# Performance work log

Hardware: AMD Instinct MI355X
Metric: run time of the kernel (lower is better)

The kernel has to match this reference:

```python
import jax, jax.numpy as jnp
import numpy as np

IN_DIM = 512
E = 512            # embed_dim
DI = 1024          # d_inner = expand * embed_dim
S = 16             # d_state
DC = 4             # d_conv
DT_RANK = 32       # ceil(embed_dim / 16)
NL = 2             # n_layers
N_SLICES = 8000
CHUNK = 500        # hard-coded batch_size in forward


def setup_inputs() -> dict:
    key = jax.random.key(0)
    ks = jax.random.split(key, 16)
    s = 0.02
    inp = {
        "slice_features": jax.random.normal(ks[0], (N_SLICES, IN_DIM), dtype=jnp.float32),
        "ip_w": jax.random.normal(ks[1], (E, IN_DIM), dtype=jnp.float32) * s,
        "ip_b": jnp.zeros((E,), jnp.float32),
        "in_ln_g": jnp.ones((E,), jnp.float32),
        "in_ln_b": jnp.zeros((E,), jnp.float32),
        "m_in_w": jax.random.normal(ks[2], (NL, 2 * DI, E), dtype=jnp.float32) * s,
        "m_conv_w": jax.random.normal(ks[3], (NL, DI, DC), dtype=jnp.float32) * s,
        "m_conv_b": jnp.zeros((NL, DI), jnp.float32),
        "m_xproj_w": jax.random.normal(ks[4], (NL, DT_RANK + 2 * S, DI), dtype=jnp.float32) * s,
        "m_dt_w": jax.random.normal(ks[5], (NL, DI, DT_RANK), dtype=jnp.float32) * s,
        "m_dt_b": jax.random.normal(ks[6], (NL, DI), dtype=jnp.float32) * 0.1,
        "m_Alog": jnp.log(jnp.tile(jnp.arange(1, S + 1, dtype=jnp.float32), (NL, DI, 1))),
        "m_D": jnp.ones((NL, DI), jnp.float32),
        "m_out_w": jax.random.normal(ks[7], (NL, E, DI), dtype=jnp.float32) * s,
        "ln_g": jnp.ones((NL, E), jnp.float32),
        "ln_b": jnp.zeros((NL, E), jnp.float32),
        "op_w": jax.random.normal(ks[8], (E, E), dtype=jnp.float32) * s,
        "op_b": jnp.zeros((E,), jnp.float32),
    }
    return inp


def _layer_norm(x, g, b):
    mu = jnp.mean(x, axis=-1, keepdims=True)
    var = jnp.mean(jnp.square(x - mu), axis=-1, keepdims=True)
    return (x - mu) * jax.lax.rsqrt(var + 1e-5) * g + b


def _mamba(h, in_w, conv_w, conv_b, xproj_w, dt_w, dt_b, Alog, Dp, out_w):
    # h: (Nc, L, E) -> (Nc, L, E)
    Nc, L, _ = h.shape
    xz = jnp.einsum('nle,de->nld', h, in_w)          # (Nc, L, 2*DI)
    x, z = jnp.split(xz, 2, axis=-1)
    # causal depthwise conv1d along L
    k = jnp.transpose(conv_w)[:, None, :]            # (DC, 1, DI) WIO grouped
    x = jax.lax.conv_general_dilated(
        x, k, window_strides=(1,), padding=[(DC - 1, 0)],
        dimension_numbers=('NWC', 'WIO', 'NWC'), feature_group_count=DI) + conv_b
    x = jax.nn.silu(x)
    x_dbl = jnp.einsum('nld,rd->nlr', x, xproj_w)    # (Nc, L, DT_RANK + 2S)
    dt = jax.nn.softplus(jnp.einsum('nlr,dr->nld', x_dbl[..., :DT_RANK], dt_w) + dt_b)
    B = x_dbl[..., DT_RANK:DT_RANK + S]
    C = x_dbl[..., DT_RANK + S:]
    A = -jnp.exp(Alog)                               # (DI, S)

    def step(hs, inp):
        dt_t, B_t, C_t, x_t = inp                    # (Nc,DI),(Nc,S),(Nc,S),(Nc,DI)
        dA = jnp.exp(dt_t[..., None] * A)            # (Nc, DI, S)
        hs = dA * hs + (dt_t * x_t)[..., None] * B_t[:, None, :]
        y = jnp.einsum('nds,ns->nd', hs, C_t)
        return hs, y

    xs = (jnp.swapaxes(dt, 0, 1), jnp.swapaxes(B, 0, 1),
          jnp.swapaxes(C, 0, 1), jnp.swapaxes(x, 0, 1))
    h0 = jnp.zeros((Nc, DI, S), dt.dtype)
    _, ys = jax.lax.scan(step, h0, xs)               # ys: (L, Nc, DI)
    y = jnp.swapaxes(ys, 0, 1) + x * Dp
    y = y * jax.nn.silu(z)
    return jnp.einsum('nld,ed->nle', y, out_w)


def reference(slice_features, ip_w, ip_b, in_ln_g, in_ln_b, m_in_w, m_conv_w, m_conv_b,
              m_xproj_w, m_dt_w, m_dt_b, m_Alog, m_D, m_out_w, ln_g, ln_b, op_w, op_b):
    h = slice_features @ ip_w.T + ip_b               # (N, E)
    h = _layer_norm(h, in_ln_g, in_ln_b)             # dropout: eval no-op
    h = h.reshape(N_SLICES // CHUNK, CHUNK, E)       # chunks of 500, batched
    for l in range(NL):
        res = h
        h = _mamba(h, m_in_w[l], m_conv_w[l], m_conv_b[l], m_xproj_w[l],
                   m_dt_w[l], m_dt_b[l], m_Alog[l], m_D[l], m_out_w[l])
        h = _layer_norm(h + res, ln_g[l], ln_b[l])
    h = h.reshape(N_SLICES, E)
    return h @ op_w.T + op_b
```

## Files before the change

### kernel.cpp

```cpp
#include <hip/hip_runtime.h>
#include <hip/hip_bf16.h>
#include <math.h>

#define NSL 8000
#define MPAD 8064
#define EDIM 512
#define DI_ 1024
#define SDIM 16
#define NLAY 2
#define CHK 500
#define PSEG 10
#define LSEG 50

typedef __bf16 bf16_t;
typedef bf16_t bf16x8 __attribute__((ext_vector_type(8)));
typedef bf16_t bf16x4 __attribute__((ext_vector_type(4)));
typedef float  f32x4  __attribute__((ext_vector_type(4)));

#define GL2LDS(g, l) __builtin_amdgcn_global_load_lds( \
    (const __attribute__((address_space(1))) void*)(g), \
    (__attribute__((address_space(3))) void*)(l), 16, 0, 0)

template<int EPI>
__global__ __launch_bounds__(256, 4)
void gemm_mfma(const bf16_t* __restrict__ Ah, const bf16_t* __restrict__ Al,
               const bf16_t* __restrict__ Wh, const bf16_t* __restrict__ Wl,
               const float* __restrict__ bias, float* __restrict__ C,
               float* __restrict__ C2, int M, int N, int K)
{
    __shared__ bf16_t sm[2 * 128 * 64];
    const int tid = threadIdx.x;
    const int w   = tid >> 6;
    const int l   = tid & 63;
    const int m0  = blockIdx.y * 128;
    const int n0  = blockIdx.x * 128;

    const int srow  = l >> 3;
    const int sslot = (l & 7) ^ srow;
    const int sc    = sslot * 8;
    const bf16_t* asrc[4];
    const bf16_t* wsrc[4];
    #pragma unroll
    for (int i = 0; i < 4; ++i) {
        const int lc  = (i << 2) | w;
        const int row = lc * 8 + srow;
        asrc[i] = (sc < 32) ? Ah + (size_t)(m0 + row) * K + sc
                            : Al + (size_t)(m0 + row) * K + (sc - 32);
        wsrc[i] = (sc < 32) ? Wh + (size_t)(n0 + row) * K + sc
                            : Wl + (size_t)(n0 + row) * K + (sc - 32);
    }

    const int wm  = (w >> 1) * 64;
    const int wn  = (w & 1) * 64;
    const int lr  = l & 15;
    const int lk  = (l >> 4) * 8;
    const int csw = (l & 7) << 3;
    const int cHi = lk ^ csw;
    const int cLo = (32 + lk) ^ csw;

    f32x4 acc[4][4];
    #pragma unroll
    for (int i = 0; i < 4; ++i)
        #pragma unroll
        for (int j = 0; j < 4; ++j) acc[i][j] = (f32x4){0.f,0.f,0.f,0.f};

    for (int kt = 0; kt < K; kt += 32) {
        #pragma unroll
        for (int i = 0; i < 4; ++i) {
            const int lc = (i << 2) | w;
            GL2LDS(asrc[i] + kt, sm + lc * 512);
            GL2LDS(wsrc[i] + kt, sm + 8192 + lc * 512);
        }
        __syncthreads();
        bf16x8 ah[4], al[4], wh[4], wl[4];
        #pragma unroll
        for (int f = 0; f < 4; ++f) {
            const int ar = (wm + f * 16 + lr) * 64;
            const int wr = (wn + f * 16 + lr) * 64;
            ah[f] = *(const bf16x8*)(sm + ar + cHi);
            al[f] = *(const bf16x8*)(sm + ar + cLo);
            wh[f] = *(const bf16x8*)(sm + 8192 + wr + cHi);
            wl[f] = *(const bf16x8*)(sm + 8192 + wr + cLo);
        }
        #pragma unroll
        for (int fi = 0; fi < 4; ++fi)
            #pragma unroll
            for (int fj = 0; fj < 4; ++fj) {
                acc[fi][fj] = __builtin_amdgcn_mfma_f32_16x16x32_bf16(ah[fi], wh[fj], acc[fi][fj], 0, 0, 0);
                acc[fi][fj] = __builtin_amdgcn_mfma_f32_16x16x32_bf16(ah[fi], wl[fj], acc[fi][fj], 0, 0, 0);
                acc[fi][fj] = __builtin_amdgcn_mfma_f32_16x16x32_bf16(al[fi], wh[fj], acc[fi][fj], 0, 0, 0);
            }
        __syncthreads();
    }
    const int r4 = (l >> 4) * 4;
    #pragma unroll
    for (int fj = 0; fj < 4; ++fj) {
        const int col = n0 + wn + fj * 16 + lr;
        if (EPI == 3 && col >= 1056) continue;
        const float bv = (EPI == 1) ? bias[col]
                       : (EPI == 3 ? (col < 1024 ? bias[col] : 0.f) : 0.f);
        #pragma unroll
        for (int fi = 0; fi < 4; ++fi) {
            const int rowb = m0 + wm + fi * 16 + r4;
            #pragma unroll
            for (int r = 0; r < 4; ++r) {
                const int row = rowb + r;
                if (row >= M) continue;
                float v = acc[fi][fj][r] + bv;
                if (EPI == 3) {
                    if (col < 1024) {
                        v = fmaxf(v, 0.f) + log1pf(__expf(-fabsf(v)));
                        C[(size_t)row * 1024 + col] = v;
                    } else {
                        C2[(size_t)row * 32 + (col - 1024)] = v;
                    }
                } else {
                    C[(size_t)row * N + col] = v;
                }
            }
        }
    }
}

__global__ __launch_bounds__(256)
void compose_dtw(const float* __restrict__ dtw,
                 const float* __restrict__ xp,
                 bf16_t* __restrict__ wh, bf16_t* __restrict__ wl)
{
    const int d0 = blockIdx.x * 4;
    const int t  = threadIdx.x;
    float acc[4][4] = {{0.f}};
    for (int r = 0; r < 32; ++r) {
        float xv[4];
        #pragma unroll
        for (int cc = 0; cc < 4; ++cc) xv[cc] = xp[r * 1024 + t + cc * 256];
        #pragma unroll
        for (int dd = 0; dd < 4; ++dd) {
            float wv = dtw[(d0 + dd) * 32 + r];
            #pragma unroll
            for (int cc = 0; cc < 4; ++cc) acc[dd][cc] = fmaf(wv, xv[cc], acc[dd][cc]);
        }
    }
    #pragma unroll
    for (int dd = 0; dd < 4; ++dd)
        #pragma unroll
        for (int cc = 0; cc < 4; ++cc) {
            float v = acc[dd][cc];
            bf16_t hb = (bf16_t)v;
            size_t o = (size_t)(d0 + dd) * 1024 + t + cc * 256;
            wh[o] = hb;
            wl[o] = (bf16_t)(v - (float)hb);
        }
}

__global__ __launch_bounds__(256)
void ln_kernel(const float* __restrict__ in, const float* __restrict__ res,
               const float* __restrict__ g, const float* __restrict__ b,
               float* __restrict__ out, bf16_t* __restrict__ oh, bf16_t* __restrict__ ol)
{
    const int lane = threadIdx.x & 63;
    const int wv = threadIdx.x >> 6;
    const int row = blockIdx.x * 4 + wv;
    const size_t base = (size_t)row * EDIM + lane * 8;
    float x[8];
    float4 v0 = *(const float4*)(in + base);
    float4 v1 = *(const float4*)(in + base + 4);
    x[0]=v0.x; x[1]=v0.y; x[2]=v0.z; x[3]=v0.w;
    x[4]=v1.x; x[5]=v1.y; x[6]=v1.z; x[7]=v1.w;
    if (res) {
        float4 r0 = *(const float4*)(res + base);
        float4 r1 = *(const float4*)(res + base + 4);
        x[0]+=r0.x; x[1]+=r0.y; x[2]+=r0.z; x[3]+=r0.w;
        x[4]+=r1.x; x[5]+=r1.y; x[6]+=r1.z; x[7]+=r1.w;
    }
    float s = 0.f, sq = 0.f;
    #pragma unroll
    for (int j = 0; j < 8; ++j) { s += x[j]; sq += x[j]*x[j]; }
    #pragma unroll
    for (int off = 32; off; off >>= 1) {
        s  += __shfl_xor(s, off);
        sq += __shfl_xor(sq, off);
    }
    float mu = s * (1.f/EDIM);
    float var = sq * (1.f/EDIM) - mu*mu;
    float rs = rsqrtf(var + 1e-5f);
    const int col = lane * 8;
    float o[8];
    bf16x8 vh, vl;
    #pragma unroll
    for (int j = 0; j < 8; ++j) {
        o[j] = (x[j] - mu) * rs * g[col+j] + b[col+j];
        bf16_t hb = (bf16_t)o[j];
        vh[j] = hb;
        vl[j] = (bf16_t)(o[j] - (float)hb);
    }
    *(float4*)(out + base)     = make_float4(o[0],o[1],o[2],o[3]);
    *(float4*)(out + base + 4) = make_float4(o[4],o[5],o[6],o[7]);
    *(bf16x8*)(oh + base) = vh;
    *(bf16x8*)(ol + base) = vl;
}

__global__ __launch_bounds__(256)
void conv_silu_k(const float* __restrict__ xz, const float* __restrict__ w,
                 const float* __restrict__ b, bf16_t* __restrict__ xch,
                 bf16_t* __restrict__ xcl)
{
    const int d  = blockIdx.x * 256 + threadIdx.x;
    const int lc = blockIdx.y;
    const int n  = blockIdx.z;
    const int l0 = lc * 100;
    const float w0 = w[d*4+0], w1 = w[d*4+1], w2 = w[d*4+2], w3 = w[d*4+3];
    const float bb = b[d];
    const float* xp = xz + (size_t)n * CHK * 2048 + d;
    float x0 = (l0-3) >= 0 ? xp[(size_t)(l0-3)*2048] : 0.f;
    float x1 = (l0-2) >= 0 ? xp[(size_t)(l0-2)*2048] : 0.f;
    float x2 = (l0-1) >= 0 ? xp[(size_t)(l0-1)*2048] : 0.f;
    const size_t ob = ((size_t)n*CHK + l0) * DI_ + d;
    for (int l = 0; l < 100; ++l) {
        float x3 = xp[(size_t)(l0+l)*2048];
        float v = fmaf(w3,x3, fmaf(w2,x2, fmaf(w1,x1, fmaf(w0,x0, bb))));
        float sv = v / (1.f + __expf(-v));
        bf16_t hv = (bf16_t)sv;
        xch[ob + (size_t)l*DI_] = hv;
        xcl[ob + (size_t)l*DI_] = (bf16_t)(sv - (float)hv);
        x0 = x1; x1 = x2; x2 = x3;
    }
}

__global__ __launch_bounds__(256)
void sc_part(const float* __restrict__ dt, const bf16_t* __restrict__ xch,
             const bf16_t* __restrict__ xcl, const float* __restrict__ bc,
             const float* __restrict__ Alog,
             float* __restrict__ pA, float* __restrict__ loc)
{
    __shared__ float Bs[LSEG][SDIM];
    const int d  = blockIdx.x * 256 + threadIdx.x;
    const int n  = blockIdx.y;
    const int sg = blockIdx.z;
    const int t0 = sg * LSEG;
    const size_t rb = (size_t)n*CHK + t0;
    for (int idx = threadIdx.x; idx < LSEG*SDIM; idx += 256) {
        int t = idx >> 4, s = idx & 15;
        Bs[t][s] = bc[(rb + t)*32 + s];
    }
    __syncthreads();
    float A[SDIM], p[SDIM], lcl[SDIM];
    #pragma unroll
    for (int s = 0; s < SDIM; ++s) {
        A[s] = -__expf(Alog[d*SDIM + s]); p[s] = 1.f; lcl[s] = 0.f;
    }
    for (int t = 0; t < LSEG; ++t) {
        float dtv = dt[(rb+t)*DI_ + d];
        float xv  = (float)xch[(rb+t)*DI_ + d] + (float)xcl[(rb+t)*DI_ + d];
        float dx = dtv * xv;
        #pragma unroll
        for (int s = 0; s < SDIM; ++s) {
            float dA = __expf(dtv * A[s]);
            p[s] *= dA;
            lcl[s] = fmaf(dA, lcl[s], dx * Bs[t][s]);
        }
    }
    const size_t ob = ((size_t)(n*PSEG + sg) << 14) + d*16;
    #pragma unroll
    for (int s = 0; s < SDIM; s += 4) {
        *(float4*)(pA  + ob + s) = make_float4(p[s],p[s+1],p[s+2],p[s+3]);
        *(float4*)(loc + ob + s) = make_float4(lcl[s],lcl[s+1],lcl[s+2],lcl[s+3]);
    }
}

__global__ __launch_bounds__(256)
void sc_comb(const float* __restrict__ pA, float* __restrict__ hio)
{
    const int gI = blockIdx.x * 256 + threadIdx.x;
    const int n = gI >> 14;
    const int r = gI & 16383;
    float h = 0.f;
    #pragma unroll
    for (int sg = 0; sg < PSEG; ++sg) {
        size_t idx = ((size_t)(n*PSEG + sg) << 14) + r;
        float pa = pA[idx];
        float lo = hio[idx];
        hio[idx] = h;
        h = fmaf(pa, h, lo);
    }
}

__global__ __launch_bounds__(256)
void sc_fin(const float* __restrict__ dt, const bf16_t* __restrict__ xch,
            const bf16_t* __restrict__ xcl, const float* __restrict__ xz,
            const float* __restrict__ bc, const float* __restrict__ Alog,
            const float* __restrict__ Dp, const float* __restrict__ hin,
            bf16_t* __restrict__ yh, bf16_t* __restrict__ yl)
{
    __shared__ float BCs[LSEG][32];
    const int d  = blockIdx.x * 256 + threadIdx.x;
    const int n  = blockIdx.y;
    const int sg = blockIdx.z;
    const int t0 = sg * LSEG;
    const size_t rb = (size_t)n*CHK + t0;
    for (int idx = threadIdx.x; idx < LSEG*32; idx += 256) {
        int t = idx >> 5, s = idx & 31;
        BCs[t][s] = bc[(rb + t)*32 + s];
    }
    __syncthreads();
    float A[SDIM], h[SDIM];
    #pragma unroll
    for (int s = 0; s < SDIM; ++s) A[s] = -__expf(Alog[d*SDIM + s]);
    const size_t hb = ((size_t)(n*PSEG + sg) << 14) + d*16;
    #pragma unroll
    for (int s = 0; s < SDIM; ++s) h[s] = hin[hb + s];
    const float Dv = Dp[d];
    for (int t = 0; t < LSEG; ++t) {
        const size_t p = rb + t;
        float dtv = dt[p*DI_ + d];
        float xv  = (float)xch[p*DI_ + d] + (float)xcl[p*DI_ + d];
        float zv  = xz[p*2048 + DI_ + d];
        float dx = dtv * xv;
        float accv = 0.f;
        #pragma unroll
        for (int s = 0; s < SDIM; ++s) {
            float dA = __expf(dtv * A[s]);
            h[s] = fmaf(dA, h[s], dx * BCs[t][s]);
            accv = fmaf(h[s], BCs[t][16+s], accv);
        }
        float yv = fmaf(xv, Dv, accv);
        float sz = zv / (1.f + __expf(-zv));
        float outv = yv * sz;
        bf16_t oh = (bf16_t)outv;
        yh[p*DI_ + d] = oh;
        yl[p*DI_ + d] = (bf16_t)(outv - (float)oh);
    }
}

__global__ __launch_bounds__(256)
void convert_split(const float* __restrict__ src, bf16_t* __restrict__ hi,
                   bf16_t* __restrict__ lo, long n, long valid)
{
    long i = ((long)blockIdx.x * 256 + threadIdx.x) * 4;
    if (i >= n) return;
    float4 v = make_float4(0.f,0.f,0.f,0.f);
    if (i < valid) v = *(const float4*)(src + i);
    float a[4] = {v.x, v.y, v.z, v.w};
    bf16x4 vh, vl;
    #pragma unroll
    for (int j = 0; j < 4; ++j) {
        bf16_t hb = (bf16_t)a[j];
        vh[j] = hb;
        vl[j] = (bf16_t)(a[j] - (float)hb);
    }
    *(bf16x4*)(hi + i) = vh;
    *(bf16x4*)(lo + i) = vl;
}

extern "C" void kernel_launch(void* const* d_in, const int* in_sizes, int n_in,
                              void* d_out, int out_size, void* d_ws, size_t ws_size,
                              hipStream_t stream) {
    (void)in_sizes; (void)n_in; (void)out_size; (void)ws_size;
    const float* sf       = (const float*)d_in[0];
    const float* ip_w     = (const float*)d_in[1];
    const float* ip_b     = (const float*)d_in[2];
    const float* ilng     = (const float*)d_in[3];
    const float* ilnb     = (const float*)d_in[4];
    const float* m_in_w   = (const float*)d_in[5];
    const float* m_conv_w = (const float*)d_in[6];
    const float* m_conv_b = (const float*)d_in[7];
    const float* m_xproj_w= (const float*)d_in[8];
    const float* m_dt_w   = (const float*)d_in[9];
    const float* m_dt_b   = (const float*)d_in[10];
    const float* m_Alog   = (const float*)d_in[11];
    const float* m_D      = (const float*)d_in[12];
    const float* m_out_w  = (const float*)d_in[13];
    const float* ln_g     = (const float*)d_in[14];
    const float* ln_b     = (const float*)d_in[15];
    const float* op_w     = (const float*)d_in[16];
    const float* op_b     = (const float*)d_in[17];
    float* outp = (float*)d_out;

    float* t0   = (float*)d_ws;
    float* h    = t0   + 4096000;
    float* xzb  = h    + 4096000;
    float* dtb  = xzb  + 16384000;
    float* bcb  = dtb  + 8192000;
    float* pAb  = bcb  + 256000;
    float* locb = pAb  + 2621440;
    bf16_t* hh  = (bf16_t*)(locb + 2621440);
    bf16_t* hl  = hh  + 4128768;
    bf16_t* xch = hl  + 4128768;
    bf16_t* xcl = xch + 8257536;
    bf16_t* yh  = xcl + 8257536;
    bf16_t* yl  = yh  + 8257536;
    bf16_t* sfh = yh;
    bf16_t* sfl = yl;
    bf16_t* wiph = yl + 8257536;
    bf16_t* wipl = wiph + 262144;
    bf16_t* winh = wipl + 262144;
    bf16_t* winl = winh + 2097152;
    bf16_t* wouth= winl + 2097152;
    bf16_t* woutl= wouth + 1048576;
    bf16_t* woph = woutl + 1048576;
    bf16_t* wopl = woph + 262144;
    bf16_t* wcmbh= wopl + 262144;
    bf16_t* wcmbl= wcmbh + 1179648;

    dim3 blk(256);
    convert_split<<<256,  blk, 0, stream>>>(ip_w,    wiph, wipl, 262144,  262144);
    convert_split<<<2048, blk, 0, stream>>>(m_in_w,  winh, winl, 2097152, 2097152);
    convert_split<<<1024, blk, 0, stream>>>(m_out_w, wouth,woutl,1048576, 1048576);
    convert_split<<<256,  blk, 0, stream>>>(op_w,    woph, wopl, 262144,  262144);
    convert_split<<<4032, blk, 0, stream>>>(sf,      sfh,  sfl,  4128768, 4096000);

    gemm_mfma<1><<<dim3(4,63), blk, 0, stream>>>(sfh, sfl, wiph, wipl, ip_b, t0, nullptr, NSL, EDIM, 512);
    ln_kernel<<<2000, blk, 0, stream>>>(t0, nullptr, ilng, ilnb, h, hh, hl);

    for (int l = 0; l < NLAY; ++l) {
        const float* xp_l  = m_xproj_w + (size_t)l * 64 * 1024;
        gemm_mfma<0><<<dim3(16,63), blk, 0, stream>>>(hh, hl, winh + (size_t)l*1048576, winl + (size_t)l*1048576,
                                                      nullptr, xzb, nullptr, NSL, 2048, EDIM);
        conv_silu_k<<<dim3(4,5,16), blk, 0, stream>>>(xzb, m_conv_w + (size_t)l*DI_*4, m_conv_b + (size_t)l*DI_, xch, xcl);
        compose_dtw<<<256, blk, 0, stream>>>(m_dt_w + (size_t)l*DI_*32, xp_l, wcmbh, wcmbl);
        convert_split<<<32, blk, 0, stream>>>(xp_l + 32*1024, wcmbh + 1048576, wcmbl + 1048576, 32768, 32768);
        gemm_mfma<3><<<dim3(9,63), blk, 0, stream>>>(xch, xcl, wcmbh, wcmbl, m_dt_b + (size_t)l*DI_,
                                                     dtb, bcb, NSL, 1152, 1024);
        sc_part<<<dim3(4,16,PSEG), blk, 0, stream>>>(dtb, xch, xcl, bcb, m_Alog + (size_t)l*DI_*SDIM, pAb, locb);
        sc_comb<<<1024, blk, 0, stream>>>(pAb, locb);
        sc_fin<<<dim3(4,16,PSEG), blk, 0, stream>>>(dtb, xch, xcl, xzb, bcb, m_Alog + (size_t)l*DI_*SDIM,
                                                    m_D + (size_t)l*DI_, locb, yh, yl);
        gemm_mfma<0><<<dim3(4,63), blk, 0, stream>>>(yh, yl, wouth + (size_t)l*524288, woutl + (size_t)l*524288,
                                                     nullptr, t0, nullptr, NSL, EDIM, DI_);
        ln_kernel<<<2000, blk, 0, stream>>>(t0, h, ln_g + (size_t)l*EDIM, ln_b + (size_t)l*EDIM, h, hh, hl);
    }
    gemm_mfma<1><<<dim3(4,63), blk, 0, stream>>>(hh, hl, woph, wopl, op_b, outp, nullptr, NSL, EDIM, 512);
}
```

Measured before the change: 918.8 us.

## Double-buffer LDS tiles in split-bf16 MFMA GEMM to overlap loads with compute

```diff
diff --git a/kernel.cpp b/kernel.cpp
--- a/kernel.cpp
+++ b/kernel.cpp
@@ -22,13 +22,13 @@
     (__attribute__((address_space(3))) void*)(l), 16, 0, 0)
 
 template<int EPI>
-__global__ __launch_bounds__(256, 4)
+__global__ __launch_bounds__(256, 2)
 void gemm_mfma(const bf16_t* __restrict__ Ah, const bf16_t* __restrict__ Al,
                const bf16_t* __restrict__ Wh, const bf16_t* __restrict__ Wl,
                const float* __restrict__ bias, float* __restrict__ C,
                float* __restrict__ C2, int M, int N, int K)
 {
-    __shared__ bf16_t sm[2 * 128 * 64];
+    __shared__ bf16_t sm[2][2 * 128 * 64];
     const int tid = threadIdx.x;
     const int w   = tid >> 6;
     const int l   = tid & 63;
@@ -64,23 +64,35 @@
         #pragma unroll
         for (int j = 0; j < 4; ++j) acc[i][j] = (f32x4){0.f,0.f,0.f,0.f};
 
-    for (int kt = 0; kt < K; kt += 32) {
+    auto stage = [&](bf16_t* dst, int kt) {
         #pragma unroll
         for (int i = 0; i < 4; ++i) {
             const int lc = (i << 2) | w;
-            GL2LDS(asrc[i] + kt, sm + lc * 512);
-            GL2LDS(wsrc[i] + kt, sm + 8192 + lc * 512);
-        }
-        __syncthreads();
+            GL2LDS(asrc[i] + kt, dst + lc * 512);
+            GL2LDS(wsrc[i] + kt, dst + 8192 + lc * 512);
+        }
+    };
+
+    stage(&sm[0][0], 0);
+    asm volatile("s_waitcnt vmcnt(0)" ::: "memory");
+    __builtin_amdgcn_s_barrier();
+    asm volatile("" ::: "memory");
+
+    const int NT = K >> 5;
+    int cur = 0;
+    for (int t = 0; t < NT; ++t) {
+        if (t + 1 < NT) stage(&sm[cur ^ 1][0], (t + 1) << 5);
+        __builtin_amdgcn_sched_barrier(0);
+        const bf16_t* smc = &sm[cur][0];
         bf16x8 ah[4], al[4], wh[4], wl[4];
         #pragma unroll
         for (int f = 0; f < 4; ++f) {
             const int ar = (wm + f * 16 + lr) * 64;
             const int wr = (wn + f * 16 + lr) * 64;
-            ah[f] = *(const bf16x8*)(sm + ar + cHi);
-            al[f] = *(const bf16x8*)(sm + ar + cLo);
-            wh[f] = *(const bf16x8*)(sm + 8192 + wr + cHi);
-            wl[f] = *(const bf16x8*)(sm + 8192 + wr + cLo);
+            ah[f] = *(const bf16x8*)(smc + ar + cHi);
+            al[f] = *(const bf16x8*)(smc + ar + cLo);
+            wh[f] = *(const bf16x8*)(smc + 8192 + wr + cHi);
+            wl[f] = *(const bf16x8*)(smc + 8192 + wr + cLo);
         }
         #pragma unroll
         for (int fi = 0; fi < 4; ++fi)
@@ -90,7 +102,10 @@
                 acc[fi][fj] = __builtin_amdgcn_mfma_f32_16x16x32_bf16(ah[fi], wl[fj], acc[fi][fj], 0, 0, 0);
                 acc[fi][fj] = __builtin_amdgcn_mfma_f32_16x16x32_bf16(al[fi], wh[fj], acc[fi][fj], 0, 0, 0);
             }
-        __syncthreads();
+        asm volatile("s_waitcnt vmcnt(0)" ::: "memory");
+        __builtin_amdgcn_s_barrier();
+        asm volatile("" ::: "memory");
+        cur ^= 1;
     }
     const int r4 = (l >> 4) * 4;
     #pragma unroll
```

Result: no change. 923.8 us (+0.5%).
